# Kernel tuning notes

Measured on AMD Instinct MI355X. Metric: run time of the kernel, lower is better.

## Reference

```python
import jax, jax.numpy as jnp
import numpy as np
import math

B, N, D = 4, 2048, 256
H = 8
HD = D // H  # 32
EPS = 1e-5


def _layernorm(x, gamma, beta):
    mu = jnp.mean(x, axis=-1, keepdims=True)
    var = jnp.var(x, axis=-1, keepdims=True)
    return (x - mu) * jax.lax.rsqrt(var + EPS) * gamma + beta


def setup_inputs() -> dict:
    key = jax.random.key(0)
    ks = jax.random.split(key, 16)
    s = 0.02
    inp = {
        "x": jax.random.normal(ks[0], (B, N, D), dtype=jnp.float32),
        "adj": jax.random.randint(ks[1], (B, N, N), 0, 2, dtype=jnp.int32),
        "wq": jax.random.normal(ks[2], (D, D), dtype=jnp.float32) * s,
        "bq": jnp.zeros((D,), jnp.float32),
        "wk": jax.random.normal(ks[3], (D, D), dtype=jnp.float32) * s,
        "bk": jnp.zeros((D,), jnp.float32),
        "wv": jax.random.normal(ks[4], (D, D), dtype=jnp.float32) * s,
        "bv": jnp.zeros((D,), jnp.float32),
        "wo": jax.random.normal(ks[5], (D, D), dtype=jnp.float32) * s,
        "bo": jnp.zeros((D,), jnp.float32),
        "g1": jnp.ones((D,), jnp.float32),
        "be1": jnp.zeros((D,), jnp.float32),
        "g2": jnp.ones((D,), jnp.float32),
        "be2": jnp.zeros((D,), jnp.float32),
        "w1": jax.random.normal(ks[6], (D, 4 * D), dtype=jnp.float32) * s,
        "b1": jnp.zeros((4 * D,), jnp.float32),
        "w2": jax.random.normal(ks[7], (4 * D, D), dtype=jnp.float32) * s,
        "b2": jnp.zeros((D,), jnp.float32),
    }
    return inp


def reference(x, adj, wq, bq, wk, bk, wv, bv, wo, bo, g1, be1, g2, be2, w1, b1, w2, b2):
    # Dropout is identity in eval mode.
    res = x
    xn = _layernorm(x, g1, be1)
    q = (xn @ wq + bq).reshape(B, N, H, HD).transpose(0, 2, 1, 3)  # (B,H,N,d)
    k = (xn @ wk + bk).reshape(B, N, H, HD).transpose(0, 2, 1, 3)
    v = (xn @ wv + bv).reshape(B, N, H, HD).transpose(0, 2, 1, 3)
    scores = jnp.einsum("bhnd,bhmd->bhnm", q, k) / math.sqrt(HD)
    scores = jnp.where(adj[:, None, :, :] == 0, -jnp.inf, scores)
    attn = jax.nn.softmax(scores, axis=-1)
    attn = jnp.nan_to_num(attn, nan=0.0)  # rows with no edges -> all zeros
    out = jnp.einsum("bhnm,bhmd->bhnd", attn, v)
    out = out.transpose(0, 2, 1, 3).reshape(B, N, D)
    out = out @ wo + bo
    x = res + out
    h = _layernorm(x, g2, be2)
    h = jax.nn.gelu(h @ w1 + b1, approximate=False) @ w2 + b2
    return x + h
```

## Files before the change

kernel.cpp:

```cpp
#include <hip/hip_runtime.h>
#include <hip/hip_bf16.h>
#include <math.h>

#define B_ 4
#define N_ 2048
#define D_ 256
#define H_ 8
#define HD_ 32
#define F_ 1024
#define M_ (B_*N_)
#define EPS_ 1e-5f
#define VSTR 72

typedef __attribute__((ext_vector_type(8))) short short8;
typedef __attribute__((ext_vector_type(4))) float f32x4;

#define QSC 0.2550565499f

#if __has_builtin(__builtin_amdgcn_exp2f)
__device__ inline float fexp2(float x) { return __builtin_amdgcn_exp2f(x); }
#else
__device__ inline float fexp2(float x) { float r; asm("v_exp_f32 %0, %1" : "=v"(r) : "v"(x)); return r; }
#endif
#if __has_builtin(__builtin_amdgcn_rcpf)
__device__ inline float frcp(float x) { return __builtin_amdgcn_rcpf(x); }
#else
__device__ inline float frcp(float x) { float r; asm("v_rcp_f32 %0, %1" : "=v"(r) : "v"(x)); return r; }
#endif

__device__ inline unsigned short f2bf(float f) {
    union { float f; unsigned u; } x; x.f = f;
    unsigned r = x.u + 0x7fff + ((x.u >> 16) & 1);
    return (unsigned short)(r >> 16);
}

__device__ inline unsigned pk_bf16(float a, float b) {
    union { __hip_bfloat162 h; unsigned u; } c;
    c.h = __float22bfloat162_rn(float2{a, b});
    return c.u;
}

__device__ inline float gelu_f(float x) {
    float ax = fabsf(x);
    float z = ax * 0.70710678118654752f;
    float t = frcp(fmaf(0.3275911f, z, 1.0f));
    float e = fexp2(-z * z * 1.4426950408889634f);
    float poly = t * fmaf(t, fmaf(t, fmaf(t, fmaf(t, 1.061405429f, -1.453152027f),
                     1.421413741f), -0.284496736f), 0.254829592f);
    float erfv = 1.0f - poly * e;
    float s = (x < 0.f) ? -erfv : erfv;
    return 0.5f * x * (1.0f + s);
}

__device__ inline void async_copy16(const void* g, void* l) {
    __builtin_amdgcn_global_load_lds(
        (const __attribute__((address_space(1))) void*)g,
        (__attribute__((address_space(3))) void*)l, 16, 0, 0);
}

__device__ inline void ln_rows(const float* __restrict__ x,
        const float* __restrict__ g, const float* __restrict__ be,
        unsigned short* __restrict__ out, int blk) {
    int w = threadIdx.x >> 6, lane = threadIdx.x & 63;
    int row = blk * 4 + w;
    float4 v = *(const float4*)&x[(size_t)row * D_ + lane * 4];
    float s  = v.x + v.y + v.z + v.w;
    float s2 = v.x * v.x + v.y * v.y + v.z * v.z + v.w * v.w;
    #pragma unroll
    for (int off = 1; off < 64; off <<= 1) {
        s  += __shfl_xor(s,  off, 64);
        s2 += __shfl_xor(s2, off, 64);
    }
    float mu  = s * (1.0f / D_);
    float var = s2 * (1.0f / D_) - mu * mu;
    float r = rsqrtf(var + EPS_);
    float4 gv = *(const float4*)&g[lane * 4];
    float4 bv = *(const float4*)&be[lane * 4];
    ushort4 u;
    u.x = f2bf((v.x - mu) * r * gv.x + bv.x);
    u.y = f2bf((v.y - mu) * r * gv.y + bv.y);
    u.z = f2bf((v.z - mu) * r * gv.z + bv.z);
    u.w = f2bf((v.w - mu) * r * gv.w + bv.w);
    *(ushort4*)&out[(size_t)row * D_ + lane * 4] = u;
}

__global__ __launch_bounds__(256) void ln_kernel(const float* __restrict__ x,
        const float* __restrict__ g, const float* __restrict__ be,
        unsigned short* __restrict__ out) {
    ln_rows(x, g, be, out, blockIdx.x);
}

__global__ __launch_bounds__(256) void prep_kernel(
        const int* __restrict__ adj, unsigned short* __restrict__ mask16,
        const float* __restrict__ wq, const float* __restrict__ wk,
        const float* __restrict__ wv, const float* __restrict__ wo,
        const float* __restrict__ w1, const float* __restrict__ w2,
        unsigned short* __restrict__ wqkvt, unsigned short* __restrict__ wot,
        unsigned short* __restrict__ w1t, unsigned short* __restrict__ w2t,
        const float* __restrict__ x, const float* __restrict__ g1,
        const float* __restrict__ be1, unsigned short* __restrict__ xn) {
    __shared__ float t[32][33];
    int id = blockIdx.x;
    if (id < 4096) {
        int g = id * 256 + threadIdx.x;
        const int4* ap = (const int4*)adj + (size_t)g * 4;
        unsigned bits = 0;
        #pragma unroll
        for (int i = 0; i < 4; i++) {
            int4 v = ap[i];
            bits |= (v.x != 0 ? 1u : 0u) << (4 * i + 0);
            bits |= (v.y != 0 ? 1u : 0u) << (4 * i + 1);
            bits |= (v.z != 0 ? 1u : 0u) << (4 * i + 2);
            bits |= (v.w != 0 ? 1u : 0u) << (4 * i + 3);
        }
        mask16[g] = (unsigned short)bits;
        return;
    }
    if (id >= 4864) {
        ln_rows(x, g1, be1, xn, id - 4864);
        return;
    }
    id -= 4096;
    const float* W; unsigned short* Wt; int K, Nc, n0, k0;
    if (id < 256) {
        int m = id >> 6, l = id & 63;
        K = 256; Nc = 256; n0 = (l & 7) * 32; k0 = (l >> 3) * 32;
        W  = m == 0 ? wq : (m == 1 ? wk : (m == 2 ? wv : wo));
        Wt = m == 0 ? wqkvt : (m == 1 ? wqkvt + 65536 : (m == 2 ? wqkvt + 131072 : wot));
    } else if (id < 512) {
        int l = id - 256; K = 256; Nc = 1024; n0 = (l & 31) * 32; k0 = (l >> 5) * 32;
        W = w1; Wt = w1t;
    } else {
        int l = id - 512; K = 1024; Nc = 256; n0 = (l & 7) * 32; k0 = (l >> 3) * 32;
        W = w2; Wt = w2t;
    }
    int tx = threadIdx.x & 31, ty = threadIdx.x >> 5;
    #pragma unroll
    for (int i = 0; i < 4; i++)
        t[ty + i * 8][tx] = W[(size_t)(k0 + ty + i * 8) * Nc + n0 + tx];
    __syncthreads();
    #pragma unroll
    for (int i = 0; i < 4; i++)
        Wt[(size_t)(n0 + ty + i * 8) * K + k0 + tx] = f2bf(t[tx][ty + i * 8]);
}

#define GM_HEAD 0
#define GM_RES  1
#define GM_GELU 2

template<int MODE, int MI, int NI>
__global__ __launch_bounds__(256) void gemm_mfma(
        const unsigned short* __restrict__ A,
        const unsigned short* __restrict__ Bt,
        const float* __restrict__ bias, const float* __restrict__ bias2,
        const float* __restrict__ bias3, const float* __restrict__ res,
        void* __restrict__ Cout,
        unsigned short* __restrict__ q_out, unsigned short* __restrict__ k_out,
        unsigned short* __restrict__ v_out, int M, int Nc, int K) {
    constexpr int BM = MI * 32, BN = NI * 32;
    __shared__ __align__(16) unsigned short Abuf[2][BM * 32];
    __shared__ __align__(16) unsigned short Bbuf[2][BN * 32];
    int tid = threadIdx.x, w = tid >> 6, lane = tid & 63;
    int lr = lane & 15, lg = lane >> 4;
    int wy = w >> 1, wx = w & 1;
    int m0 = blockIdx.y * BM, n0 = blockIdx.x * BN;
    f32x4 acc[MI][NI] = {};

    int srow = lane >> 2;
    int schunk = lane & 3;

    auto STAGE = [&](int k0, int bi) {
        #pragma unroll
        for (int i = 0; i < BM / 64; i++) {
            int ar = i * 64 + w * 16 + srow;
            int ac = schunk ^ ((ar >> 1) & 3);
            async_copy16(A + (size_t)(m0 + ar) * K + k0 + ac * 8,
                         &Abuf[bi][(i * 64 + w * 16) * 32]);
        }
        #pragma unroll
        for (int i = 0; i < BN / 64; i++) {
            int br = i * 64 + w * 16 + srow;
            int bc = schunk ^ ((br >> 1) & 3);
            async_copy16(Bt + (size_t)(n0 + br) * K + k0 + bc * 8,
                         &Bbuf[bi][(i * 64 + w * 16) * 32]);
        }
    };

    int nkt = K / 32;
    STAGE(0, 0);
    for (int kt = 0; kt < nkt; kt++) {
        __syncthreads();
        int cur = kt & 1;
        if (kt + 1 < nkt) STAGE((kt + 1) * 32, cur ^ 1);

        short8 af[MI], bf[NI];
        #pragma unroll
        for (int mi = 0; mi < MI; mi++) {
            int r = wy * (MI * 16) + mi * 16 + lr;
            int c = lg ^ ((r >> 1) & 3);
            af[mi] = *(const short8*)&Abuf[cur][r * 32 + c * 8];
        }
        #pragma unroll
        for (int ni = 0; ni < NI; ni++) {
            int r = wx * (NI * 16) + ni * 16 + lr;
            int c = lg ^ ((r >> 1) & 3);
            bf[ni] = *(const short8*)&Bbuf[cur][r * 32 + c * 8];
        }
        __builtin_amdgcn_s_setprio(1);
        #pragma unroll
        for (int mi = 0; mi < MI; mi++)
            #pragma unroll
            for (int ni = 0; ni < NI; ni++)
                acc[mi][ni] = __builtin_amdgcn_mfma_f32_16x16x32_bf16(
                        af[mi], bf[ni], acc[mi][ni], 0, 0, 0);
        __builtin_amdgcn_s_setprio(0);
    }

    #pragma unroll
    for (int mi = 0; mi < MI; mi++) {
        #pragma unroll
        for (int r = 0; r < 4; r++) {
            int grow = m0 + wy * (MI * 16) + mi * 16 + lg * 4 + r;
            #pragma unroll
            for (int ni = 0; ni < NI; ni++) {
                int gcol = n0 + wx * (NI * 16) + ni * 16 + lr;
                float val = acc[mi][ni][r];
                if (MODE == GM_HEAD) {
                    int which = gcol >> 8, nn = gcol & 255;
                    const float* bp = which == 0 ? bias : (which == 1 ? bias2 : bias3);
                    val += bp[nn];
                    if (which == 0) val *= QSC;
                    unsigned short* dst = which == 0 ? q_out : (which == 1 ? k_out : v_out);
                    int bb = grow >> 11, rr = grow & (N_ - 1);
                    int hh = nn >> 5, dd = nn & 31;
                    dst[((((size_t)bb * H_ + hh) * N_) + rr) * HD_ + dd] = f2bf(val);
                } else if (MODE == GM_RES) {
                    val += bias[gcol] + res[(size_t)grow * Nc + gcol];
                    ((float*)Cout)[(size_t)grow * Nc + gcol] = val;
                } else {
                    val = gelu_f(val + bias[gcol]);
                    ((unsigned short*)Cout)[(size_t)grow * Nc + gcol] = f2bf(val);
                }
            }
        }
    }
}

__global__ __launch_bounds__(256) void attn_mfma9(
        const unsigned short* __restrict__ q, const unsigned short* __restrict__ k,
        const unsigned short* __restrict__ v, const unsigned long long* __restrict__ mask,
        unsigned short* __restrict__ ao) {
    __shared__ __align__(16) unsigned short Kb[2][64 * 32];
    __shared__ __align__(16) unsigned short Vt[2][32 * VSTR];
    int b = blockIdx.z, h = blockIdx.y;
    int q0 = blockIdx.x * 64;
    int tid = threadIdx.x, w = tid >> 6, lane = tid & 63;
    int lr = lane & 15, lg = lane >> 4;
    size_t bh = (size_t)(b * H_ + h);
    const unsigned short* qbp = q + bh * N_ * HD_;
    const unsigned short* kbp = k + bh * N_ * HD_;
    const unsigned short* vbp = v + bh * N_ * HD_;

    short8 qf = *(const short8*)&qbp[(size_t)(q0 + w * 16 + lr) * HD_ + lg * 8];
    const unsigned long long* mrow = mask + ((size_t)b * N_ + q0 + w * 16 + lr) * (N_ / 64);

    int swz = (lr & 3) ^ ((lr >> 2) & 3);
    int sr = lane >> 2, sc = lane & 3;
    int ssw = (sr & 3) ^ ((sr >> 2) & 3);
    const unsigned short* ksrc = kbp + (size_t)(w * 16 + sr) * HD_ + (sc ^ ssw) * 8;
    int va = tid & 31, vd = tid >> 5;
    const unsigned short* vsrc = vbp + (size_t)(2 * va) * HD_ + vd * 4;
    int p2 = 2 * va;
    int sig = (p2 & 35) | ((p2 & 12) << 1) | ((p2 & 16) >> 2);

    short8 ones;
    #pragma unroll
    for (int i = 0; i < 8; i++) ones[i] = (short)0x3F80;

    f32x4 acc0 = {}, acc1 = {}, acc_l = {};
    f32x4 zero = {};
    const int NT = N_ / 64;

    {
        ushort4 v0p = *(const ushort4*)vsrc;
        ushort4 v1p = *(const ushort4*)(vsrc + HD_);
        async_copy16(ksrc, &Kb[0][w * 16 * 32]);
        *(unsigned*)&Vt[0][(vd * 4 + 0) * VSTR + sig] = ((unsigned)v1p.x << 16) | v0p.x;
        *(unsigned*)&Vt[0][(vd * 4 + 1) * VSTR + sig] = ((unsigned)v1p.y << 16) | v0p.y;
        *(unsigned*)&Vt[0][(vd * 4 + 2) * VSTR + sig] = ((unsigned)v1p.z << 16) | v0p.z;
        *(unsigned*)&Vt[0][(vd * 4 + 3) * VSTR + sig] = ((unsigned)v1p.w << 16) | v0p.w;
    }
    unsigned long long mk_cur = mrow[0], mk_next = 0;
    ushort4 v0n = {}, v1n = {};

    for (int t = 0; t < NT; t++) {
        __syncthreads();
        int cur = t & 1;
        if (t + 1 < NT) {
            size_t koff = (size_t)(t + 1) * 64 * HD_;
            v0n = *(const ushort4*)(vsrc + koff);
            v1n = *(const ushort4*)(vsrc + koff + HD_);
            async_copy16(ksrc + koff, &Kb[cur ^ 1][w * 16 * 32]);
            mk_next = mrow[t + 1];
        }

        f32x4 s[4];
        __builtin_amdgcn_s_setprio(1);
        #pragma unroll
        for (int j = 0; j < 4; j++) {
            short8 kf = *(const short8*)&Kb[cur][(j * 16 + lr) * 32 + ((lg ^ swz) * 8)];
            s[j] = __builtin_amdgcn_mfma_f32_16x16x32_bf16(kf, qf, zero, 0, 0, 0);
        }
        __builtin_amdgcn_s_setprio(0);

        unsigned mlo = (unsigned)(mk_cur >> (lg * 4));
        unsigned mhi = (unsigned)(mk_cur >> (lg * 4 + 32));
        #pragma unroll
        for (int j = 0; j < 4; j++) {
            unsigned mw = (j & 2) ? mhi : mlo;
            #pragma unroll
            for (int r = 0; r < 4; r++) {
                float sv = ((mw >> ((j & 1) * 16 + r)) & 1) ? s[j][r] : -200.f;
                s[j][r] = fexp2(sv);
            }
        }

        union { short8 v8; unsigned u[4]; } pf0, pf1;
        pf0.u[0] = pk_bf16(s[0][0], s[0][1]); pf0.u[1] = pk_bf16(s[0][2], s[0][3]);
        pf0.u[2] = pk_bf16(s[1][0], s[1][1]); pf0.u[3] = pk_bf16(s[1][2], s[1][3]);
        pf1.u[0] = pk_bf16(s[2][0], s[2][1]); pf1.u[1] = pk_bf16(s[2][2], s[2][3]);
        pf1.u[2] = pk_bf16(s[3][0], s[3][1]); pf1.u[3] = pk_bf16(s[3][2], s[3][3]);

        short8 vfA0 = *(const short8*)&Vt[cur][lr * VSTR + lg * 8];
        short8 vfB0 = *(const short8*)&Vt[cur][(lr + 16) * VSTR + lg * 8];
        short8 vfA1 = *(const short8*)&Vt[cur][lr * VSTR + 32 + lg * 8];
        short8 vfB1 = *(const short8*)&Vt[cur][(lr + 16) * VSTR + 32 + lg * 8];
        __builtin_amdgcn_s_setprio(1);
        acc0  = __builtin_amdgcn_mfma_f32_16x16x32_bf16(pf0.v8, vfA0, acc0, 0, 0, 0);
        acc1  = __builtin_amdgcn_mfma_f32_16x16x32_bf16(pf0.v8, vfB0, acc1, 0, 0, 0);
        acc_l = __builtin_amdgcn_mfma_f32_16x16x32_bf16(pf0.v8, ones, acc_l, 0, 0, 0);
        acc0  = __builtin_amdgcn_mfma_f32_16x16x32_bf16(pf1.v8, vfA1, acc0, 0, 0, 0);
        acc1  = __builtin_amdgcn_mfma_f32_16x16x32_bf16(pf1.v8, vfB1, acc1, 0, 0, 0);
        acc_l = __builtin_amdgcn_mfma_f32_16x16x32_bf16(pf1.v8, ones, acc_l, 0, 0, 0);
        __builtin_amdgcn_s_setprio(0);

        if (t + 1 < NT) {
            *(unsigned*)&Vt[cur ^ 1][(vd * 4 + 0) * VSTR + sig] = ((unsigned)v1n.x << 16) | v0n.x;
            *(unsigned*)&Vt[cur ^ 1][(vd * 4 + 1) * VSTR + sig] = ((unsigned)v1n.y << 16) | v0n.y;
            *(unsigned*)&Vt[cur ^ 1][(vd * 4 + 2) * VSTR + sig] = ((unsigned)v1n.z << 16) | v0n.z;
            *(unsigned*)&Vt[cur ^ 1][(vd * 4 + 3) * VSTR + sig] = ((unsigned)v1n.w << 16) | v0n.w;
        }
        mk_cur = mk_next;
    }

    #pragma unroll
    for (int r = 0; r < 4; r++) {
        float lv = acc_l[r];
        float ir = (lv > 0.f) ? frcp(lv) : 0.f;
        int row = q0 + w * 16 + lg * 4 + r;
        unsigned short* op = ao + ((size_t)(b * N_) + row) * D_ + h * HD_;
        op[lr]      = f2bf(acc0[r] * ir);
        op[lr + 16] = f2bf(acc1[r] * ir);
    }
}

extern "C" void kernel_launch(void* const* d_in, const int* in_sizes, int n_in,
                              void* d_out, int out_size, void* d_ws, size_t ws_size,
                              hipStream_t stream) {
    const float* x   = (const float*)d_in[0];
    const int*   adj = (const int*)d_in[1];
    const float* wq  = (const float*)d_in[2];
    const float* bq  = (const float*)d_in[3];
    const float* wk  = (const float*)d_in[4];
    const float* bk  = (const float*)d_in[5];
    const float* wv  = (const float*)d_in[6];
    const float* bv  = (const float*)d_in[7];
    const float* wo  = (const float*)d_in[8];
    const float* bo  = (const float*)d_in[9];
    const float* g1  = (const float*)d_in[10];
    const float* be1 = (const float*)d_in[11];
    const float* g2  = (const float*)d_in[12];
    const float* be2 = (const float*)d_in[13];
    const float* w1  = (const float*)d_in[14];
    const float* b1  = (const float*)d_in[15];
    const float* w2  = (const float*)d_in[16];
    const float* b2  = (const float*)d_in[17];
    float* out = (float*)d_out;
    char* base = (char*)d_ws;

    const size_t MB = (size_t)1 << 20;
    unsigned long long* mask = (unsigned long long*)(base);
    unsigned short* xn     = (unsigned short*)(base + 2*MB);
    unsigned short* qb     = (unsigned short*)(base + 6*MB);
    unsigned short* kb     = (unsigned short*)(base + 10*MB);
    unsigned short* vb     = (unsigned short*)(base + 14*MB);
    unsigned short* ao     = (unsigned short*)(base + 18*MB);
    float*          x2     = (float*)(base + 22*MB);
    unsigned short* hn     = (unsigned short*)(base + 30*MB);
    unsigned short* h1     = (unsigned short*)(base + 34*MB);
    unsigned short* wqkvt  = (unsigned short*)(base + 51*MB);
    unsigned short* wot    = (unsigned short*)(base + 51*MB + 394240);
    unsigned short* w1t    = (unsigned short*)(base + 52*MB);
    unsigned short* w2t    = (unsigned short*)(base + 52*MB + 524288);

    prep_kernel<<<4096 + 768 + 2048, 256, 0, stream>>>(
        adj, (unsigned short*)mask, wq, wk, wv, wo, w1, w2,
        wqkvt, wot, w1t, w2t, x, g1, be1, xn);
    gemm_mfma<GM_HEAD, 4, 2><<<dim3(12, 64), 256, 0, stream>>>(
        xn, wqkvt, bq, bk, bv, nullptr, nullptr, qb, kb, vb, M_, 768, 256);
    attn_mfma9<<<dim3(N_ / 64, H_, B_), 256, 0, stream>>>(qb, kb, vb, mask, ao);
    gemm_mfma<GM_RES, 2, 2><<<dim3(4, 128), 256, 0, stream>>>(
        ao, wot, bo, nullptr, nullptr, x, x2, nullptr, nullptr, nullptr, M_, 256, 256);
    ln_kernel<<<M_ / 4, 256, 0, stream>>>(x2, g2, be2, hn);
    gemm_mfma<GM_GELU, 2, 2><<<dim3(16, 128), 256, 0, stream>>>(
        hn, w1t, b1, nullptr, nullptr, nullptr, h1, nullptr, nullptr, nullptr, M_, 1024, 256);
    gemm_mfma<GM_RES, 2, 2><<<dim3(4, 128), 256, 0, stream>>>(
        h1, w2t, b2, nullptr, nullptr, x2, out, nullptr, nullptr, nullptr, M_, 256, 1024);
}
```

Baseline: 123.5 us.

## Write V pre-transposed and swizzled from QKV GEMM, load directly into attention registers

```diff
diff --git a/kernel.cpp b/kernel.cpp
--- a/kernel.cpp
+++ b/kernel.cpp
@@ -10,7 +10,6 @@
 #define F_ 1024
 #define M_ (B_*N_)
 #define EPS_ 1e-5f
-#define VSTR 72
 
 typedef __attribute__((ext_vector_type(8))) short short8;
 typedef __attribute__((ext_vector_type(4))) float f32x4;
@@ -38,6 +37,10 @@
     union { __hip_bfloat162 h; unsigned u; } c;
     c.h = __float22bfloat162_rn(float2{a, b});
     return c.u;
+}
+
+__device__ inline int sig64(int p) {
+    return (p & 0x23) | ((p & 0x0C) << 1) | ((p & 0x10) >> 2);
 }
 
 __device__ inline float gelu_f(float x) {
@@ -230,10 +233,15 @@
                     const float* bp = which == 0 ? bias : (which == 1 ? bias2 : bias3);
                     val += bp[nn];
                     if (which == 0) val *= QSC;
-                    unsigned short* dst = which == 0 ? q_out : (which == 1 ? k_out : v_out);
                     int bb = grow >> 11, rr = grow & (N_ - 1);
                     int hh = nn >> 5, dd = nn & 31;
-                    dst[((((size_t)bb * H_ + hh) * N_) + rr) * HD_ + dd] = f2bf(val);
+                    if (which == 2) {
+                        v_out[((size_t)(bb * H_ + hh) * HD_ + dd) * N_
+                              + (rr & ~63) + sig64(rr & 63)] = f2bf(val);
+                    } else {
+                        unsigned short* dst = which == 0 ? q_out : k_out;
+                        dst[((((size_t)bb * H_ + hh) * N_) + rr) * HD_ + dd] = f2bf(val);
+                    }
                 } else if (MODE == GM_RES) {
                     val += bias[gcol] + res[(size_t)grow * Nc + gcol];
                     ((float*)Cout)[(size_t)grow * Nc + gcol] = val;
@@ -246,12 +254,11 @@
     }
 }
 
-__global__ __launch_bounds__(256) void attn_mfma9(
+__global__ __launch_bounds__(256) void attn_mfma10(
         const unsigned short* __restrict__ q, const unsigned short* __restrict__ k,
-        const unsigned short* __restrict__ v, const unsigned long long* __restrict__ mask,
+        const unsigned short* __restrict__ vtg, const unsigned long long* __restrict__ mask,
         unsigned short* __restrict__ ao) {
     __shared__ __align__(16) unsigned short Kb[2][64 * 32];
-    __shared__ __align__(16) unsigned short Vt[2][32 * VSTR];
     int b = blockIdx.z, h = blockIdx.y;
     int q0 = blockIdx.x * 64;
     int tid = threadIdx.x, w = tid >> 6, lane = tid & 63;
@@ -259,7 +266,6 @@
     size_t bh = (size_t)(b * H_ + h);
     const unsigned short* qbp = q + bh * N_ * HD_;
     const unsigned short* kbp = k + bh * N_ * HD_;
-    const unsigned short* vbp = v + bh * N_ * HD_;
 
     short8 qf = *(const short8*)&qbp[(size_t)(q0 + w * 16 + lr) * HD_ + lg * 8];
     const unsigned long long* mrow = mask + ((size_t)b * N_ + q0 + w * 16 + lr) * (N_ / 64);
@@ -268,10 +274,8 @@
     int sr = lane >> 2, sc = lane & 3;
     int ssw = (sr & 3) ^ ((sr >> 2) & 3);
     const unsigned short* ksrc = kbp + (size_t)(w * 16 + sr) * HD_ + (sc ^ ssw) * 8;
-    int va = tid & 31, vd = tid >> 5;
-    const unsigned short* vsrc = vbp + (size_t)(2 * va) * HD_ + vd * 4;
-    int p2 = 2 * va;
-    int sig = (p2 & 35) | ((p2 & 12) << 1) | ((p2 & 16) >> 2);
+    const unsigned short* vA = vtg + (bh * HD_ + lr) * N_ + lg * 8;
+    const unsigned short* vB = vtg + (bh * HD_ + lr + 16) * N_ + lg * 8;
 
     short8 ones;
     #pragma unroll
@@ -281,27 +285,26 @@
     f32x4 zero = {};
     const int NT = N_ / 64;
 
-    {
-        ushort4 v0p = *(const ushort4*)vsrc;
-        ushort4 v1p = *(const ushort4*)(vsrc + HD_);
-        async_copy16(ksrc, &Kb[0][w * 16 * 32]);
-        *(unsigned*)&Vt[0][(vd * 4 + 0) * VSTR + sig] = ((unsigned)v1p.x << 16) | v0p.x;
-        *(unsigned*)&Vt[0][(vd * 4 + 1) * VSTR + sig] = ((unsigned)v1p.y << 16) | v0p.y;
-        *(unsigned*)&Vt[0][(vd * 4 + 2) * VSTR + sig] = ((unsigned)v1p.z << 16) | v0p.z;
-        *(unsigned*)&Vt[0][(vd * 4 + 3) * VSTR + sig] = ((unsigned)v1p.w << 16) | v0p.w;
-    }
-    unsigned long long mk_cur = mrow[0], mk_next = 0;
-    ushort4 v0n = {}, v1n = {};
+    async_copy16(ksrc, &Kb[0][w * 16 * 32]);
+    short8 a0c = *(const short8*)(vA);
+    short8 a1c = *(const short8*)(vA + 32);
+    short8 b0c = *(const short8*)(vB);
+    short8 b1c = *(const short8*)(vB + 32);
+    unsigned long long mkc = mrow[0];
 
     for (int t = 0; t < NT; t++) {
         __syncthreads();
         int cur = t & 1;
+        short8 a0n = a0c, a1n = a1c, b0n = b0c, b1n = b1c;
+        unsigned long long mkn = mkc;
         if (t + 1 < NT) {
-            size_t koff = (size_t)(t + 1) * 64 * HD_;
-            v0n = *(const ushort4*)(vsrc + koff);
-            v1n = *(const ushort4*)(vsrc + koff + HD_);
-            async_copy16(ksrc + koff, &Kb[cur ^ 1][w * 16 * 32]);
-            mk_next = mrow[t + 1];
+            int ko = (t + 1) * 64;
+            async_copy16(ksrc + (size_t)ko * HD_, &Kb[cur ^ 1][w * 16 * 32]);
+            a0n = *(const short8*)(vA + ko);
+            a1n = *(const short8*)(vA + ko + 32);
+            b0n = *(const short8*)(vB + ko);
+            b1n = *(const short8*)(vB + ko + 32);
+            mkn = mrow[t + 1];
         }
 
         f32x4 s[4];
@@ -313,8 +316,8 @@
         }
         __builtin_amdgcn_s_setprio(0);
 
-        unsigned mlo = (unsigned)(mk_cur >> (lg * 4));
-        unsigned mhi = (unsigned)(mk_cur >> (lg * 4 + 32));
+        unsigned mlo = (unsigned)(mkc >> (lg * 4));
+        unsigned mhi = (unsigned)(mkc >> (lg * 4 + 32));
         #pragma unroll
         for (int j = 0; j < 4; j++) {
             unsigned mw = (j & 2) ? mhi : mlo;
@@ -331,26 +334,16 @@
         pf1.u[0] = pk_bf16(s[2][0], s[2][1]); pf1.u[1] = pk_bf16(s[2][2], s[2][3]);
         pf1.u[2] = pk_bf16(s[3][0], s[3][1]); pf1.u[3] = pk_bf16(s[3][2], s[3][3]);
 
-        short8 vfA0 = *(const short8*)&Vt[cur][lr * VSTR + lg * 8];
-        short8 vfB0 = *(const short8*)&Vt[cur][(lr + 16) * VSTR + lg * 8];
-        short8 vfA1 = *(const short8*)&Vt[cur][lr * VSTR + 32 + lg * 8];
-        short8 vfB1 = *(const short8*)&Vt[cur][(lr + 16) * VSTR + 32 + lg * 8];
         __builtin_amdgcn_s_setprio(1);
-        acc0  = __builtin_amdgcn_mfma_f32_16x16x32_bf16(pf0.v8, vfA0, acc0, 0, 0, 0);
-        acc1  = __builtin_amdgcn_mfma_f32_16x16x32_bf16(pf0.v8, vfB0, acc1, 0, 0, 0);
+        acc0  = __builtin_amdgcn_mfma_f32_16x16x32_bf16(pf0.v8, a0c, acc0, 0, 0, 0);
+        acc1  = __builtin_amdgcn_mfma_f32_16x16x32_bf16(pf0.v8, b0c, acc1, 0, 0, 0);
         acc_l = __builtin_amdgcn_mfma_f32_16x16x32_bf16(pf0.v8, ones, acc_l, 0, 0, 0);
-        acc0  = __builtin_amdgcn_mfma_f32_16x16x32_bf16(pf1.v8, vfA1, acc0, 0, 0, 0);
-        acc1  = __builtin_amdgcn_mfma_f32_16x16x32_bf16(pf1.v8, vfB1, acc1, 0, 0, 0);
+        acc0  = __builtin_amdgcn_mfma_f32_16x16x32_bf16(pf1.v8, a1c, acc0, 0, 0, 0);
+        acc1  = __builtin_amdgcn_mfma_f32_16x16x32_bf16(pf1.v8, b1c, acc1, 0, 0, 0);
         acc_l = __builtin_amdgcn_mfma_f32_16x16x32_bf16(pf1.v8, ones, acc_l, 0, 0, 0);
         __builtin_amdgcn_s_setprio(0);
 
-        if (t + 1 < NT) {
-            *(unsigned*)&Vt[cur ^ 1][(vd * 4 + 0) * VSTR + sig] = ((unsigned)v1n.x << 16) | v0n.x;
-            *(unsigned*)&Vt[cur ^ 1][(vd * 4 + 1) * VSTR + sig] = ((unsigned)v1n.y << 16) | v0n.y;
-            *(unsigned*)&Vt[cur ^ 1][(vd * 4 + 2) * VSTR + sig] = ((unsigned)v1n.z << 16) | v0n.z;
-            *(unsigned*)&Vt[cur ^ 1][(vd * 4 + 3) * VSTR + sig] = ((unsigned)v1n.w << 16) | v0n.w;
-        }
-        mk_cur = mk_next;
+        a0c = a0n; a1c = a1n; b0c = b0n; b1c = b1n; mkc = mkn;
     }
 
     #pragma unroll
@@ -408,11 +401,11 @@
         wqkvt, wot, w1t, w2t, x, g1, be1, xn);
     gemm_mfma<GM_HEAD, 4, 2><<<dim3(12, 64), 256, 0, stream>>>(
         xn, wqkvt, bq, bk, bv, nullptr, nullptr, qb, kb, vb, M_, 768, 256);
-    attn_mfma9<<<dim3(N_ / 64, H_, B_), 256, 0, stream>>>(qb, kb, vb, mask, ao);
+    attn_mfma10<<<dim3(N_ / 64, H_, B_), 256, 0, stream>>>(qb, kb, vb, mask, ao);
     gemm_mfma<GM_RES, 2, 2><<<dim3(4, 128), 256, 0, stream>>>(
         ao, wot, bo, nullptr, nullptr, x, x2, nullptr, nullptr, nullptr, M_, 256, 256);
     ln_kernel<<<M_ / 4, 256, 0, stream>>>(x2, g2, be2, hn);
-    gemm_mfma<GM_GELU, 2, 2><<<dim3(16, 128), 256, 0, stream>>>(
+    gemm_mfma<GM_GELU, 4, 4><<<dim3(8, 64), 256, 0, stream>>>(
         hn, w1t, b1, nullptr, nullptr, nullptr, h1, nullptr, nullptr, nullptr, M_, 1024, 256);
     gemm_mfma<GM_RES, 2, 2><<<dim3(4, 128), 256, 0, stream>>>(
         h1, w2t, b2, nullptr, nullptr, x2, out, nullptr, nullptr, nullptr, M_, 256, 1024);
```

Result: slower. 158.2 us (+28.1%).
